# Optimization experiments

Measured on AMD Instinct MI355X. Metric: run time of the kernel, lower is better.

The kernel has to match this reference:

```python
import jax, jax.numpy as jnp
import numpy as np

D_MODEL = 1024
N_HEADS = 16
EPS = 1e-6


def setup_inputs() -> dict:
    key = jax.random.key(0)
    k1, k2, k3 = jax.random.split(key, 3)
    B, T, D = 2, 2048, D_MODEL
    x = jax.random.normal(k1, (B, T, D), dtype=jnp.float32)
    # learned params
    norm_weight = jnp.ones((D,), dtype=jnp.float32)
    qkv_w = jax.random.normal(k2, (3 * D, D), dtype=jnp.float32) * (1.0 / np.sqrt(D))
    out_w = jax.random.normal(k3, (D, D), dtype=jnp.float32) * (1.0 / np.sqrt(D))
    return {"x": x, "norm_weight": norm_weight, "qkv_w": qkv_w, "out_w": out_w}


def reference(x, norm_weight, qkv_w, out_w):
    B, T, D = x.shape
    H = N_HEADS
    d = D // H
    # RMSNorm
    ms = jnp.mean(x * x, axis=-1, keepdims=True)
    xn = x * jax.lax.rsqrt(ms + EPS) * norm_weight
    # QKV projection (Linear, no bias): y = x @ W^T
    qkv = jnp.einsum('btd,ed->bte', xn, qkv_w)  # (B,T,3D)
    q, k, v = jnp.split(qkv, 3, axis=-1)
    q = q.reshape(B, T, H, d)
    k = k.reshape(B, T, H, d)
    v = v.reshape(B, T, H, d)
    # scores (B,H,T,T) with causal mask
    scores = jnp.einsum('bqhd,bkhd->bhqk', q, k) / np.sqrt(d).astype(np.float32)
    causal = jnp.tril(jnp.ones((T, T), dtype=bool))
    scores = jnp.where(causal[None, None], scores, -jnp.inf)
    probs = jax.nn.softmax(scores, axis=-1)
    ctx = jnp.einsum('bhqk,bkhd->bqhd', probs, v)  # (B,T,H,d)
    out = ctx.reshape(B, T, D)
    out = jnp.einsum('btd,ed->bte', out, out_w)
    return out
```

## Files before the change

kernel.cpp:

```cpp
#include <hip/hip_runtime.h>
#include <stdint.h>

#define B_SZ 2
#define T_SZ 2048
#define DMODEL 1024
#define HCNT 16
#define HD 64
#define MROWS (B_SZ * T_SZ)

typedef __attribute__((ext_vector_type(8))) __bf16 bf16x8;
typedef __attribute__((ext_vector_type(4))) __bf16 bf16x4;
typedef __attribute__((ext_vector_type(4))) float f32x4;
typedef __attribute__((ext_vector_type(8))) unsigned short u16x8;

__device__ __forceinline__ unsigned short f2bf(float f) {
  union { float f; uint32_t u; } v; v.f = f;
  uint32_t u = v.u;
  u += 0x7fffu + ((u >> 16) & 1u);
  return (unsigned short)(u >> 16);
}

__device__ __forceinline__ void gld_lds16(const void* g, void* l) {
  __builtin_amdgcn_global_load_lds((__attribute__((address_space(1))) void*)(uintptr_t)g,
                                   (__attribute__((address_space(3))) void*)l, 16, 0, 0);
}

__global__ __launch_bounds__(256)
void cvt_bf16(const float* __restrict__ in, unsigned short* __restrict__ out, int n4) {
  int i = blockIdx.x * 256 + threadIdx.x;
  if (i >= n4) return;
  float4 v = ((const float4*)in)[i];
  ushort4 o;
  o.x = f2bf(v.x); o.y = f2bf(v.y); o.z = f2bf(v.z); o.w = f2bf(v.w);
  ((ushort4*)out)[i] = o;
}

__global__ __launch_bounds__(256)
void rmsnorm_bf16(const float* __restrict__ x, const float* __restrict__ w,
                  unsigned short* __restrict__ xn) {
  const int row = blockIdx.x;
  const int t = threadIdx.x;
  float4 v = ((const float4*)(x + (size_t)row * DMODEL))[t];
  float ss = v.x * v.x + v.y * v.y + v.z * v.z + v.w * v.w;
#pragma unroll
  for (int o = 1; o < 64; o <<= 1) ss += __shfl_xor(ss, o, 64);
  __shared__ float red[4];
  if ((t & 63) == 0) red[t >> 6] = ss;
  __syncthreads();
  float tot = red[0] + red[1] + red[2] + red[3];
  float scale = rsqrtf(tot * (1.0f / (float)DMODEL) + 1e-6f);
  float4 wv = ((const float4*)w)[t];
  ushort4 o;
  o.x = f2bf(v.x * scale * wv.x);
  o.y = f2bf(v.y * scale * wv.y);
  o.z = f2bf(v.z * scale * wv.z);
  o.w = f2bf(v.w * scale * wv.w);
  ((ushort4*)(xn + (size_t)row * DMODEL))[t] = o;
}

__device__ __forceinline__ void stage128x32(const unsigned short* g, int ldg,
                                            unsigned short* lds, int wave, int lane) {
#pragma unroll
  for (int i = 0; i < 2; ++i) {
    const unsigned short* gp = g + (size_t)(i * 64 + wave * 16 + (lane >> 2)) * ldg + (lane & 3) * 8;
    gld_lds16(gp, lds + i * 2048 + wave * 512);
  }
}

template <int F32OUT>
__global__ __launch_bounds__(256, 2)
void gemm_bt(const unsigned short* __restrict__ A, const unsigned short* __restrict__ B,
             void* __restrict__ Cv, int M, int N, int K) {
  __shared__ __align__(16) unsigned short As[2][128 * 32];
  __shared__ __align__(16) unsigned short Bs[2][128 * 32];
  const int t = threadIdx.x, wave = t >> 6, lane = t & 63;
  const int m0 = blockIdx.y * 128, n0 = blockIdx.x * 128;
  const int wr = wave >> 1, wc = wave & 1;
  f32x4 acc[4][4] = {};
  const int nk = K >> 5;
  stage128x32(A + (size_t)m0 * K, K, As[0], wave, lane);
  stage128x32(B + (size_t)n0 * K, K, Bs[0], wave, lane);
  __syncthreads();
  int buf = 0;
  for (int kt = 0; kt < nk; ++kt) {
    if (kt + 1 < nk) {
      stage128x32(A + (size_t)m0 * K + (kt + 1) * 32, K, As[buf ^ 1], wave, lane);
      stage128x32(B + (size_t)n0 * K + (kt + 1) * 32, K, Bs[buf ^ 1], wave, lane);
    }
    bf16x8 af[4], bfr[4];
#pragma unroll
    for (int mi = 0; mi < 4; ++mi)
      af[mi] = *(const bf16x8*)&As[buf][(wr * 64 + mi * 16 + (lane & 15)) * 32 + (lane >> 4) * 8];
#pragma unroll
    for (int ni = 0; ni < 4; ++ni)
      bfr[ni] = *(const bf16x8*)&Bs[buf][(wc * 64 + ni * 16 + (lane & 15)) * 32 + (lane >> 4) * 8];
#pragma unroll
    for (int mi = 0; mi < 4; ++mi)
#pragma unroll
      for (int ni = 0; ni < 4; ++ni)
        acc[mi][ni] = __builtin_amdgcn_mfma_f32_16x16x32_bf16(af[mi], bfr[ni], acc[mi][ni], 0, 0, 0);
    __syncthreads();
    buf ^= 1;
  }
  const int cr = (lane >> 4) * 4, cc = lane & 15;
#pragma unroll
  for (int mi = 0; mi < 4; ++mi)
#pragma unroll
    for (int ni = 0; ni < 4; ++ni) {
      int row = m0 + wr * 64 + mi * 16 + cr;
      int col = n0 + wc * 64 + ni * 16 + cc;
      if (F32OUT) {
        float* C = (float*)Cv;
#pragma unroll
        for (int r = 0; r < 4; ++r) C[(size_t)(row + r) * N + col] = acc[mi][ni][r];
      } else {
        unsigned short* C = (unsigned short*)Cv;
#pragma unroll
        for (int r = 0; r < 4; ++r) C[(size_t)(row + r) * N + col] = f2bf(acc[mi][ni][r]);
      }
    }
}

__global__ __launch_bounds__(256, 2)
void attn_causal(const unsigned short* __restrict__ qkv, unsigned short* __restrict__ ctx) {
  __shared__ __align__(16) unsigned short Ks[2][64 * 64];
  __shared__ __align__(16) unsigned short Vt[2][64 * 72];
  __shared__ __align__(16) unsigned short Pl[4][32 * 72];
  const int tid = threadIdx.x, wave = tid >> 6, lane = tid & 63;
  const int id = blockIdx.x;
  const int bh = (id & 7) + 8 * ((id >> 3) & 3);
  const int m = id >> 5;
  const int qt = (m < 8) ? (15 - m) : (m - 8);
  const int b = bh >> 4, h = bh & 15;
  const int q0 = qt * 128 + wave * 32;
  const size_t base = (size_t)b * T_SZ * 3 * DMODEL;
  const int koffK = DMODEL + h * HD;
  const int koffV = 2 * DMODEL + h * HD;
  const int nkb = 2 * (qt + 1);
  const int c = lane & 15, qg = lane >> 4;

  bf16x8 aq[2][2];
#pragma unroll
  for (int mi = 0; mi < 2; ++mi)
#pragma unroll
    for (int kk = 0; kk < 2; ++kk) {
      int q = q0 + mi * 16 + c;
      aq[mi][kk] = *(const bf16x8*)(qkv + base + (size_t)q * 3 * DMODEL + h * HD + kk * 32 + qg * 8);
    }

  float mst[2] = {-3e38f, -3e38f}, lst[2] = {0.f, 0.f};
  f32x4 aco[2][4];
#pragma unroll
  for (int mi = 0; mi < 2; ++mi)
#pragma unroll
    for (int nd = 0; nd < 4; ++nd)
#pragma unroll
      for (int r = 0; r < 4; ++r) aco[mi][nd][r] = 0.f;

  const int kr = tid >> 3;
  const int kc = tid & 7;

  auto stageK = [&](int kb, int bufi) {
#pragma unroll
    for (int i = 0; i < 2; ++i) {
      int row = i * 32 + kr;
      gld_lds16(qkv + base + (size_t)(kb + row) * 3 * DMODEL + koffK + ((kc ^ (row & 7)) << 3),
                &Ks[bufi][i * 2048 + (wave << 9)]);
    }
  };
  auto loadV = [&](int kb, u16x8* v) {
#pragma unroll
    for (int i = 0; i < 2; ++i)
      v[i] = *(const u16x8*)(qkv + base + (size_t)(kb + i * 32 + kr) * 3 * DMODEL + koffV + kc * 8);
  };
  auto writeV = [&](int bufi, const u16x8* v) {
#pragma unroll
    for (int i = 0; i < 2; ++i) {
      int kv = i * 32 + kr;
#pragma unroll
      for (int j = 0; j < 8; ++j) {
        int dd = kc * 8 + j;
        int f = ((dd >> 3) ^ dd) & 7;
        Vt[bufi][dd * 72 + ((((kv >> 3) ^ f) << 3) | (kv & 7))] = v[i][j];
      }
    }
  };

  auto computeTile = [&](int kb, int bufi) {
    f32x4 s[4][2] = {};
#pragma unroll
    for (int kk = 0; kk < 2; ++kk) {
      bf16x8 bk[4];
#pragma unroll
      for (int ni = 0; ni < 4; ++ni) {
        int row = ni * 16 + c;
        int crd = kk * 4 + qg;
        bk[ni] = *(const bf16x8*)&Ks[bufi][row * 64 + ((crd ^ (row & 7)) << 3)];
      }
#pragma unroll
      for (int ni = 0; ni < 4; ++ni)
#pragma unroll
        for (int mi = 0; mi < 2; ++mi)
          s[ni][mi] = __builtin_amdgcn_mfma_f32_16x16x32_bf16(bk[ni], aq[mi][kk], s[ni][mi], 0, 0, 0);
    }
    const bool domask = (kb + 63 > q0);
#pragma unroll
    for (int ni = 0; ni < 4; ++ni)
#pragma unroll
      for (int mi = 0; mi < 2; ++mi)
#pragma unroll
        for (int r = 0; r < 4; ++r) {
          float v = s[ni][mi][r] * 0.125f;
          if (domask) {
            int kg = kb + ni * 16 + qg * 4 + r;
            int qq = q0 + mi * 16 + c;
            if (kg > qq) v = -1e30f;
          }
          s[ni][mi][r] = v;
        }
    float crr[2][4];
#pragma unroll
    for (int mi = 0; mi < 2; ++mi) {
      float rm = -3e38f;
#pragma unroll
      for (int ni = 0; ni < 4; ++ni)
#pragma unroll
        for (int r = 0; r < 4; ++r) rm = fmaxf(rm, s[ni][mi][r]);
      rm = fmaxf(rm, __shfl_xor(rm, 16, 64));
      rm = fmaxf(rm, __shfl_xor(rm, 32, 64));
      float mo = mst[mi];
      float mn = fmaxf(mo, rm);
      float corr = __expf(mo - mn);
      float rs = 0.f;
#pragma unroll
      for (int ni = 0; ni < 4; ++ni)
#pragma unroll
        for (int r = 0; r < 4; ++r) {
          float p = __expf(s[ni][mi][r] - mn);
          s[ni][mi][r] = p;
          rs += p;
        }
      rs += __shfl_xor(rs, 16, 64);
      rs += __shfl_xor(rs, 32, 64);
      lst[mi] = lst[mi] * corr + rs;
      mst[mi] = mn;
#pragma unroll
      for (int r = 0; r < 4; ++r)
        crr[mi][r] = __shfl(corr, qg * 20 + r, 64);
    }
#pragma unroll
    for (int mi = 0; mi < 2; ++mi)
#pragma unroll
      for (int nd = 0; nd < 4; ++nd)
#pragma unroll
        for (int r = 0; r < 4; ++r) aco[mi][nd][r] *= crr[mi][r];
    unsigned short* P = Pl[wave];
#pragma unroll
    for (int ni = 0; ni < 4; ++ni)
#pragma unroll
      for (int mi = 0; mi < 2; ++mi) {
        bf16x4 pk;
#pragma unroll
        for (int r = 0; r < 4; ++r) pk[r] = (__bf16)s[ni][mi][r];
        *(bf16x4*)&P[(mi * 16 + c) * 72 + ni * 16 + qg * 4] = pk;
      }
#pragma unroll
    for (int kk = 0; kk < 2; ++kk) {
      bf16x8 pa[2], bv[4];
#pragma unroll
      for (int mi = 0; mi < 2; ++mi)
        pa[mi] = *(const bf16x8*)&P[(mi * 16 + c) * 72 + kk * 32 + qg * 8];
#pragma unroll
      for (int nd = 0; nd < 4; ++nd) {
        int dd = nd * 16 + c;
        int f = ((dd >> 3) ^ dd) & 7;
        int crd = kk * 4 + qg;
        bv[nd] = *(const bf16x8*)&Vt[bufi][dd * 72 + ((crd ^ f) << 3)];
      }
#pragma unroll
      for (int mi = 0; mi < 2; ++mi)
#pragma unroll
        for (int nd = 0; nd < 4; ++nd)
          aco[mi][nd] = __builtin_amdgcn_mfma_f32_16x16x32_bf16(pa[mi], bv[nd], aco[mi][nd], 0, 0, 0);
    }
  };

  stageK(0, 0);
  u16x8 v0[2];
  loadV(0, v0);
  writeV(0, v0);
  __syncthreads();
  int buf = 0;
  for (int t = 0; t < nkb; ++t) {
    const int kb = t * 64;
    const bool hn = (t + 1 < nkb);
    u16x8 vn[2];
    if (hn) { stageK(kb + 64, buf ^ 1); loadV(kb + 64, vn); }
    if (kb <= q0 + 31) computeTile(kb, buf);
    if (hn) writeV(buf ^ 1, vn);
    __syncthreads();
    buf ^= 1;
  }

  unsigned short* outp = ctx + (size_t)b * T_SZ * DMODEL + h * HD;
#pragma unroll
  for (int mi = 0; mi < 2; ++mi) {
    float linv = 1.f / lst[mi];
#pragma unroll
    for (int r = 0; r < 4; ++r) {
      float inv = __shfl(linv, qg * 20 + r, 64);
      int q = q0 + mi * 16 + qg * 4 + r;
#pragma unroll
      for (int nd = 0; nd < 4; ++nd)
        outp[(size_t)q * DMODEL + nd * 16 + c] = f2bf(aco[mi][nd][r] * inv);
    }
  }
}

extern "C" void kernel_launch(void* const* d_in, const int* in_sizes, int n_in,
                              void* d_out, int out_size, void* d_ws, size_t ws_size,
                              hipStream_t stream) {
  const float* x = (const float*)d_in[0];
  const float* nw = (const float*)d_in[1];
  const float* qkv_w = (const float*)d_in[2];
  const float* out_w = (const float*)d_in[3];
  float* out = (float*)d_out;

  unsigned short* ws = (unsigned short*)d_ws;
  unsigned short* xn = ws;
  unsigned short* qkvw = xn + (size_t)MROWS * DMODEL;
  unsigned short* outw = qkvw + (size_t)3 * DMODEL * DMODEL;
  unsigned short* qkv = outw + (size_t)DMODEL * DMODEL;
  unsigned short* ctx = qkv + (size_t)MROWS * 3 * DMODEL;

  cvt_bf16<<<dim3(3 * DMODEL * DMODEL / 1024), dim3(256), 0, stream>>>(qkv_w, qkvw, 3 * DMODEL * DMODEL / 4);
  cvt_bf16<<<dim3(DMODEL * DMODEL / 1024), dim3(256), 0, stream>>>(out_w, outw, DMODEL * DMODEL / 4);
  rmsnorm_bf16<<<dim3(MROWS), dim3(256), 0, stream>>>(x, nw, xn);
  gemm_bt<0><<<dim3(3 * DMODEL / 128, MROWS / 128), dim3(256), 0, stream>>>(xn, qkvw, qkv, MROWS, 3 * DMODEL, DMODEL);
  attn_causal<<<dim3(512), dim3(256), 0, stream>>>(qkv, ctx);
  gemm_bt<1><<<dim3(DMODEL / 128, MROWS / 128), dim3(256), 0, stream>>>(ctx, outw, out, MROWS, DMODEL, DMODEL);
}
```

Before: 137.0 us.

## Enlarge attention KV tiles, add lazy rescale and exp2, fuse weight casts, swizzle GEMM grid

The attention kernel now processes 128-key tiles per iteration. It folds the softmax scale and log2e into Q so it can use exp2, and it rescales the running max only when the new max exceeds the old one by a threshold. MFMA phases get raised wave priority. The two weight-conversion kernels are merged into one launch, and both GEMMs use a 1D grid with an XCD-style block swizzle to improve L2 locality. The risks are extra LDS use and a second barrier per attention iteration, wasted work on masked diagonal tiles, and a small precision change from rounding the pre-scaled Q to bf16.

```diff
diff --git a/kernel.cpp b/kernel.cpp
--- a/kernel.cpp
+++ b/kernel.cpp
@@ -20,19 +20,28 @@
   return (unsigned short)(u >> 16);
 }
 
+__device__ __forceinline__ float fexp2(float x) {
+#if __has_builtin(__builtin_amdgcn_exp2f)
+  return __builtin_amdgcn_exp2f(x);
+#else
+  return exp2f(x);
+#endif
+}
+
 __device__ __forceinline__ void gld_lds16(const void* g, void* l) {
   __builtin_amdgcn_global_load_lds((__attribute__((address_space(1))) void*)(uintptr_t)g,
                                    (__attribute__((address_space(3))) void*)l, 16, 0, 0);
 }
 
 __global__ __launch_bounds__(256)
-void cvt_bf16(const float* __restrict__ in, unsigned short* __restrict__ out, int n4) {
+void cvt_all(const float* __restrict__ qkv_w, const float* __restrict__ out_w,
+             unsigned short* __restrict__ dst) {
   int i = blockIdx.x * 256 + threadIdx.x;
-  if (i >= n4) return;
-  float4 v = ((const float4*)in)[i];
+  const int n1 = 3 * DMODEL * DMODEL / 4;
+  float4 v = (i < n1) ? ((const float4*)qkv_w)[i] : ((const float4*)out_w)[i - n1];
   ushort4 o;
   o.x = f2bf(v.x); o.y = f2bf(v.y); o.z = f2bf(v.z); o.w = f2bf(v.w);
-  ((ushort4*)out)[i] = o;
+  ((ushort4*)dst)[i] = o;
 }
 
 __global__ __launch_bounds__(256)
@@ -70,11 +79,13 @@
 template <int F32OUT>
 __global__ __launch_bounds__(256, 2)
 void gemm_bt(const unsigned short* __restrict__ A, const unsigned short* __restrict__ B,
-             void* __restrict__ Cv, int M, int N, int K) {
+             void* __restrict__ Cv, int M, int N, int K, int nbx) {
   __shared__ __align__(16) unsigned short As[2][128 * 32];
   __shared__ __align__(16) unsigned short Bs[2][128 * 32];
   const int t = threadIdx.x, wave = t >> 6, lane = t & 63;
-  const int m0 = blockIdx.y * 128, n0 = blockIdx.x * 128;
+  const int cpx = gridDim.x >> 3;
+  const int swz = (blockIdx.x & 7) * cpx + (blockIdx.x >> 3);
+  const int m0 = (swz / nbx) * 128, n0 = (swz % nbx) * 128;
   const int wr = wave >> 1, wc = wave & 1;
   f32x4 acc[4][4] = {};
   const int nk = K >> 5;
@@ -123,29 +134,33 @@
 
 __global__ __launch_bounds__(256, 2)
 void attn_causal(const unsigned short* __restrict__ qkv, unsigned short* __restrict__ ctx) {
-  __shared__ __align__(16) unsigned short Ks[2][64 * 64];
+  __shared__ __align__(16) unsigned short Ks[2][128 * 64];
   __shared__ __align__(16) unsigned short Vt[2][64 * 72];
   __shared__ __align__(16) unsigned short Pl[4][32 * 72];
   const int tid = threadIdx.x, wave = tid >> 6, lane = tid & 63;
   const int id = blockIdx.x;
   const int bh = (id & 7) + 8 * ((id >> 3) & 3);
-  const int m = id >> 5;
-  const int qt = (m < 8) ? (15 - m) : (m - 8);
+  const int p = id >> 5;
+  const int qt = (p < 8) ? (15 - p) : (p - 8);
   const int b = bh >> 4, h = bh & 15;
   const int q0 = qt * 128 + wave * 32;
   const size_t base = (size_t)b * T_SZ * 3 * DMODEL;
   const int koffK = DMODEL + h * HD;
   const int koffV = 2 * DMODEL + h * HD;
-  const int nkb = 2 * (qt + 1);
+  const int nit = qt + 1;
   const int c = lane & 15, qg = lane >> 4;
 
+  const float QSC = 0.125f * 1.4426950408889634f;
   bf16x8 aq[2][2];
 #pragma unroll
   for (int mi = 0; mi < 2; ++mi)
 #pragma unroll
     for (int kk = 0; kk < 2; ++kk) {
       int q = q0 + mi * 16 + c;
-      aq[mi][kk] = *(const bf16x8*)(qkv + base + (size_t)q * 3 * DMODEL + h * HD + kk * 32 + qg * 8);
+      bf16x8 f = *(const bf16x8*)(qkv + base + (size_t)q * 3 * DMODEL + h * HD + kk * 32 + qg * 8);
+#pragma unroll
+      for (int j = 0; j < 8; ++j) f[j] = (__bf16)((float)f[j] * QSC);
+      aq[mi][kk] = f;
     }
 
   float mst[2] = {-3e38f, -3e38f}, lst[2] = {0.f, 0.f};
@@ -162,7 +177,7 @@
 
   auto stageK = [&](int kb, int bufi) {
 #pragma unroll
-    for (int i = 0; i < 2; ++i) {
+    for (int i = 0; i < 4; ++i) {
       int row = i * 32 + kr;
       gld_lds16(qkv + base + (size_t)(kb + row) * 3 * DMODEL + koffK + ((kc ^ (row & 7)) << 3),
                 &Ks[bufi][i * 2048 + (wave << 9)]);
@@ -170,136 +185,149 @@
   };
   auto loadV = [&](int kb, u16x8* v) {
 #pragma unroll
-    for (int i = 0; i < 2; ++i)
+    for (int i = 0; i < 4; ++i)
       v[i] = *(const u16x8*)(qkv + base + (size_t)(kb + i * 32 + kr) * 3 * DMODEL + koffV + kc * 8);
   };
-  auto writeV = [&](int bufi, const u16x8* v) {
-#pragma unroll
-    for (int i = 0; i < 2; ++i) {
-      int kv = i * 32 + kr;
+  auto writeV = [&](const u16x8* v) {
+#pragma unroll
+    for (int i = 0; i < 4; ++i) {
+      int ch = i >> 1;
+      int kv = (i & 1) * 32 + kr;
 #pragma unroll
       for (int j = 0; j < 8; ++j) {
         int dd = kc * 8 + j;
-        int f = ((dd >> 3) ^ dd) & 7;
-        Vt[bufi][dd * 72 + ((((kv >> 3) ^ f) << 3) | (kv & 7))] = v[i][j];
+        int f = kc ^ j;
+        Vt[ch][dd * 72 + ((((kv >> 3) ^ f) << 3) | (kv & 7))] = v[i][j];
       }
     }
   };
 
-  auto computeTile = [&](int kb, int bufi) {
-    f32x4 s[4][2] = {};
+  auto computeTile = [&](int kb, int kbuf) {
+    f32x4 s[8][2] = {};
+    __builtin_amdgcn_s_setprio(1);
 #pragma unroll
     for (int kk = 0; kk < 2; ++kk) {
-      bf16x8 bk[4];
-#pragma unroll
-      for (int ni = 0; ni < 4; ++ni) {
+      bf16x8 bk[8];
+#pragma unroll
+      for (int ni = 0; ni < 8; ++ni) {
         int row = ni * 16 + c;
         int crd = kk * 4 + qg;
-        bk[ni] = *(const bf16x8*)&Ks[bufi][row * 64 + ((crd ^ (row & 7)) << 3)];
-      }
-#pragma unroll
-      for (int ni = 0; ni < 4; ++ni)
+        bk[ni] = *(const bf16x8*)&Ks[kbuf][row * 64 + ((crd ^ (row & 7)) << 3)];
+      }
+#pragma unroll
+      for (int ni = 0; ni < 8; ++ni)
 #pragma unroll
         for (int mi = 0; mi < 2; ++mi)
           s[ni][mi] = __builtin_amdgcn_mfma_f32_16x16x32_bf16(bk[ni], aq[mi][kk], s[ni][mi], 0, 0, 0);
     }
-    const bool domask = (kb + 63 > q0);
-#pragma unroll
-    for (int ni = 0; ni < 4; ++ni)
-#pragma unroll
-      for (int mi = 0; mi < 2; ++mi)
-#pragma unroll
-        for (int r = 0; r < 4; ++r) {
-          float v = s[ni][mi][r] * 0.125f;
-          if (domask) {
+    __builtin_amdgcn_s_setprio(0);
+    if (kb + 127 > q0) {
+#pragma unroll
+      for (int ni = 0; ni < 8; ++ni)
+#pragma unroll
+        for (int mi = 0; mi < 2; ++mi)
+#pragma unroll
+          for (int r = 0; r < 4; ++r) {
             int kg = kb + ni * 16 + qg * 4 + r;
             int qq = q0 + mi * 16 + c;
-            if (kg > qq) v = -1e30f;
+            if (kg > qq) s[ni][mi][r] = -1e30f;
           }
-          s[ni][mi][r] = v;
-        }
-    float crr[2][4];
+    }
 #pragma unroll
     for (int mi = 0; mi < 2; ++mi) {
       float rm = -3e38f;
 #pragma unroll
-      for (int ni = 0; ni < 4; ++ni)
+      for (int ni = 0; ni < 8; ++ni)
 #pragma unroll
         for (int r = 0; r < 4; ++r) rm = fmaxf(rm, s[ni][mi][r]);
       rm = fmaxf(rm, __shfl_xor(rm, 16, 64));
       rm = fmaxf(rm, __shfl_xor(rm, 32, 64));
       float mo = mst[mi];
-      float mn = fmaxf(mo, rm);
-      float corr = __expf(mo - mn);
+      float mn = mo;
+      if (__any(rm > mo + 11.5f)) {
+        mn = fmaxf(mo, rm);
+        float corr = fexp2(mo - mn);
+        lst[mi] *= corr;
+        mst[mi] = mn;
+#pragma unroll
+        for (int r = 0; r < 4; ++r) {
+          float cr = __shfl(corr, qg * 20 + r, 64);
+#pragma unroll
+          for (int nd = 0; nd < 4; ++nd) aco[mi][nd][r] *= cr;
+        }
+      }
       float rs = 0.f;
 #pragma unroll
-      for (int ni = 0; ni < 4; ++ni)
+      for (int ni = 0; ni < 8; ++ni)
 #pragma unroll
         for (int r = 0; r < 4; ++r) {
-          float p = __expf(s[ni][mi][r] - mn);
-          s[ni][mi][r] = p;
-          rs += p;
+          float pv = fexp2(s[ni][mi][r] - mn);
+          s[ni][mi][r] = pv;
+          rs += pv;
         }
       rs += __shfl_xor(rs, 16, 64);
       rs += __shfl_xor(rs, 32, 64);
-      lst[mi] = lst[mi] * corr + rs;
-      mst[mi] = mn;
-#pragma unroll
-      for (int r = 0; r < 4; ++r)
-        crr[mi][r] = __shfl(corr, qg * 20 + r, 64);
-    }
-#pragma unroll
-    for (int mi = 0; mi < 2; ++mi)
-#pragma unroll
-      for (int nd = 0; nd < 4; ++nd)
-#pragma unroll
-        for (int r = 0; r < 4; ++r) aco[mi][nd][r] *= crr[mi][r];
+      lst[mi] += rs;
+    }
     unsigned short* P = Pl[wave];
 #pragma unroll
-    for (int ni = 0; ni < 4; ++ni)
-#pragma unroll
-      for (int mi = 0; mi < 2; ++mi) {
-        bf16x4 pk;
-#pragma unroll
-        for (int r = 0; r < 4; ++r) pk[r] = (__bf16)s[ni][mi][r];
-        *(bf16x4*)&P[(mi * 16 + c) * 72 + ni * 16 + qg * 4] = pk;
-      }
-#pragma unroll
-    for (int kk = 0; kk < 2; ++kk) {
-      bf16x8 pa[2], bv[4];
-#pragma unroll
-      for (int mi = 0; mi < 2; ++mi)
-        pa[mi] = *(const bf16x8*)&P[(mi * 16 + c) * 72 + kk * 32 + qg * 8];
-#pragma unroll
-      for (int nd = 0; nd < 4; ++nd) {
-        int dd = nd * 16 + c;
-        int f = ((dd >> 3) ^ dd) & 7;
-        int crd = kk * 4 + qg;
-        bv[nd] = *(const bf16x8*)&Vt[bufi][dd * 72 + ((crd ^ f) << 3)];
-      }
-#pragma unroll
-      for (int mi = 0; mi < 2; ++mi)
-#pragma unroll
-        for (int nd = 0; nd < 4; ++nd)
-          aco[mi][nd] = __builtin_amdgcn_mfma_f32_16x16x32_bf16(pa[mi], bv[nd], aco[mi][nd], 0, 0, 0);
+    for (int ch = 0; ch < 2; ++ch) {
+      if (ch == 1) {
+        asm volatile("s_waitcnt lgkmcnt(0)" ::: "memory");
+        __builtin_amdgcn_sched_barrier(0);
+      }
+#pragma unroll
+      for (int n2 = 0; n2 < 4; ++n2) {
+        int ni = ch * 4 + n2;
+#pragma unroll
+        for (int mi = 0; mi < 2; ++mi) {
+          bf16x4 pk;
+#pragma unroll
+          for (int r = 0; r < 4; ++r) pk[r] = (__bf16)s[ni][mi][r];
+          *(bf16x4*)&P[(mi * 16 + c) * 72 + n2 * 16 + qg * 4] = pk;
+        }
+      }
+      __builtin_amdgcn_s_setprio(1);
+#pragma unroll
+      for (int kk = 0; kk < 2; ++kk) {
+        bf16x8 pa[2], bv[4];
+#pragma unroll
+        for (int mi = 0; mi < 2; ++mi)
+          pa[mi] = *(const bf16x8*)&P[(mi * 16 + c) * 72 + kk * 32 + qg * 8];
+#pragma unroll
+        for (int nd = 0; nd < 4; ++nd) {
+          int dd = nd * 16 + c;
+          int f = ((dd >> 3) ^ dd) & 7;
+          int crd = kk * 4 + qg;
+          bv[nd] = *(const bf16x8*)&Vt[ch][dd * 72 + ((crd ^ f) << 3)];
+        }
+#pragma unroll
+        for (int mi = 0; mi < 2; ++mi)
+#pragma unroll
+          for (int nd = 0; nd < 4; ++nd)
+            aco[mi][nd] = __builtin_amdgcn_mfma_f32_16x16x32_bf16(pa[mi], bv[nd], aco[mi][nd], 0, 0, 0);
+      }
+      __builtin_amdgcn_s_setprio(0);
     }
   };
 
   stageK(0, 0);
-  u16x8 v0[2];
+  u16x8 v0[4];
   loadV(0, v0);
-  writeV(0, v0);
   __syncthreads();
-  int buf = 0;
-  for (int t = 0; t < nkb; ++t) {
-    const int kb = t * 64;
-    const bool hn = (t + 1 < nkb);
-    u16x8 vn[2];
-    if (hn) { stageK(kb + 64, buf ^ 1); loadV(kb + 64, vn); }
-    if (kb <= q0 + 31) computeTile(kb, buf);
-    if (hn) writeV(buf ^ 1, vn);
+  writeV(v0);
+  __syncthreads();
+  int kbuf = 0;
+  for (int t = 0; t < nit; ++t) {
+    const int kb = t * 128;
+    const bool hn = (t + 1 < nit);
+    u16x8 vn[4];
+    if (hn) { stageK(kb + 128, kbuf ^ 1); loadV(kb + 128, vn); }
+    computeTile(kb, kbuf);
     __syncthreads();
-    buf ^= 1;
+    if (hn) writeV(vn);
+    __syncthreads();
+    kbuf ^= 1;
   }
 
   unsigned short* outp = ctx + (size_t)b * T_SZ * DMODEL + h * HD;
@@ -333,10 +361,9 @@
   unsigned short* qkv = outw + (size_t)DMODEL * DMODEL;
   unsigned short* ctx = qkv + (size_t)MROWS * 3 * DMODEL;
 
-  cvt_bf16<<<dim3(3 * DMODEL * DMODEL / 1024), dim3(256), 0, stream>>>(qkv_w, qkvw, 3 * DMODEL * DMODEL / 4);
-  cvt_bf16<<<dim3(DMODEL * DMODEL / 1024), dim3(256), 0, stream>>>(out_w, outw, DMODEL * DMODEL / 4);
+  cvt_all<<<dim3(4096), dim3(256), 0, stream>>>(qkv_w, out_w, qkvw);
   rmsnorm_bf16<<<dim3(MROWS), dim3(256), 0, stream>>>(x, nw, xn);
-  gemm_bt<0><<<dim3(3 * DMODEL / 128, MROWS / 128), dim3(256), 0, stream>>>(xn, qkvw, qkv, MROWS, 3 * DMODEL, DMODEL);
+  gemm_bt<0><<<dim3(768), dim3(256), 0, stream>>>(xn, qkvw, qkv, MROWS, 3 * DMODEL, DMODEL, 24);
   attn_causal<<<dim3(512), dim3(256), 0, stream>>>(qkv, ctx);
-  gemm_bt<1><<<dim3(DMODEL / 128, MROWS / 128), dim3(256), 0, stream>>>(ctx, outw, out, MROWS, DMODEL, DMODEL);
-}
+  gemm_bt<1><<<dim3(256), dim3(256), 0, stream>>>(ctx, outw, out, MROWS, DMODEL, DMODEL, 8);
+}
```

New measurement: 121.1 us. 1.13x faster.
